# Kernel optimization log

Hardware: AMD Instinct MI355X
Metric: run time of the kernel (lower is better)

Reference implementation:

```python
import jax, jax.numpy as jnp
import numpy as np

N, C, H, W = 4, 256, 128, 128
BLOCK = 8
FWB = H // BLOCK  # feature_size_with_block = 16
N_BBOX = 100
M = N_BBOX * N * FWB * FWB  # 102400 rois


def setup_inputs() -> dict:
    key = jax.random.key(0)
    ks = jax.random.split(key, 6)
    s = 1.0 / np.sqrt(C).astype(np.float32)
    return {
        "feature": jax.random.normal(ks[0], (N, C, H, W), jnp.float32),
        "rois_feature": jax.random.normal(ks[1], (M, C, 1, 1), jnp.float32),
        "W_weight": jax.random.normal(ks[2], (C, C), jnp.float32) * s,
        "b_weight": jnp.zeros((C,), jnp.float32),
        "W_fuse": jax.random.normal(ks[3], (C, C), jnp.float32) * s,
        "b_fuse": jnp.zeros((C,), jnp.float32),
        "W_pw": jax.random.normal(ks[4], (BLOCK * BLOCK, C), jnp.float32) * s,
        "b_pw": jnp.zeros((BLOCK * BLOCK,), jnp.float32),
        "feature_size_with_block": FWB,
    }


def reference(feature, rois_feature, W_weight, b_weight, W_fuse, b_fuse, W_pw, b_pw, feature_size_with_block):
    n, c, h, w = feature.shape
    f = feature_size_with_block
    blk = h // f  # block_size
    m = rois_feature.shape[0]
    n_bbox = m // (n * f * f)

    x = rois_feature[:, :, 0, 0]  # [M, C] (1x1 conv on 1x1 spatial == dense layer)
    feat_w = jax.nn.relu(x @ W_weight.T + b_weight)  # [M, C]
    feat_f = jax.nn.relu(x @ W_fuse.T + b_fuse)      # [M, C]
    point_weight = feat_w @ W_pw.T + b_pw            # [M, B*B]

    # [n_bbox, N, F, F, B, B] -> [N, n_bbox, F, F, B, B]
    pw = point_weight.reshape(n_bbox, n, f, f, blk, blk).transpose(1, 0, 2, 3, 4, 5)
    # feature -> blocks: [N, C, F, B, F, B] -> [N, C, F, F, B, B]
    fb = feature.reshape(n, c, f, blk, f, blk).transpose(0, 1, 2, 4, 3, 5)
    # weighted block-sum without materializing the n_bbox-repeated tensor.
    # torch: sum over (B,B) -> [N,nb,C,F,F], then permute(1,0,3,4,2) -> [nb,N,F,F,C]
    out = jnp.einsum('ncpqab,nkpqab->knpqc', fb, pw)  # [nb, N, F, F, C]
    out = out.reshape(m, c)[:, :, None, None]          # [M, C, 1, 1]
    fused = feat_f[:, :, None, None] + out
    return fused, out
```

## Files before the change

### kernel.cpp

```cpp
#include <hip/hip_runtime.h>

#define NN 4
#define CC 256
#define HH 128
#define FWBv 16
#define BLK 8
#define NBBOX 100
#define MM (NBBOX * NN * FWBv * FWBv)

typedef __attribute__((ext_vector_type(8))) short bf16x8;
typedef __attribute__((ext_vector_type(4))) float f32x4;

__device__ __forceinline__ unsigned short f2bf(float x) {
  union { float f; unsigned int u; } v; v.f = x;
  unsigned int r = v.u + 0x7FFFu + ((v.u >> 16) & 1u);
  return (unsigned short)(r >> 16);
}

__device__ __forceinline__ void async16(const void* g, void* l) {
  __builtin_amdgcn_global_load_lds(
      (__attribute__((address_space(1))) void*)(g),
      (__attribute__((address_space(3))) void*)(l), 16, 0, 0);
}

__global__ __launch_bounds__(256) void k_convert(
    const float* __restrict__ Wf, const float* __restrict__ Ww,
    const float* __restrict__ Wpw,
    unsigned short* __restrict__ oWf, unsigned short* __restrict__ oWw,
    unsigned short* __restrict__ oWpw) {
  int i = blockIdx.x * 256 + threadIdx.x;
  oWf[i] = f2bf(Wf[i]);
  oWw[i] = f2bf(Ww[i]);
  if (i < 64 * 256) oWpw[i] = f2bf(Wpw[i]);
}


__device__ __forceinline__ void stage_w(const unsigned short* __restrict__ Wp,
                                        int kc, unsigned short* buf, int w,
                                        int lane) {
  const int srcs = ((lane & 3) ^ ((lane >> 3) & 3)) * 8;
  const int rr = lane >> 2;
#pragma unroll
  for (int i = 0; i < 4; ++i) {
    const int r0 = w * 64 + i * 16;
    async16(Wp + (size_t)(r0 + rr) * 256 + kc * 32 + srcs, buf + r0 * 32);
  }
}

__device__ __forceinline__ void stage_wpw(const unsigned short* __restrict__ Wpw,
                                          unsigned short* buf, int kc4, int w,
                                          int lane) {
  const int srcs = ((lane & 7) ^ ((lane >> 3) & 7)) * 8;
  const int rr = lane >> 3;
#pragma unroll
  for (int i = 0; i < 2; ++i) {
    const int r0 = w * 16 + i * 8;
    async16(Wpw + (size_t)(r0 + rr) * 256 + kc4 * 64 + srcs, buf + r0 * 64);
  }
}

__device__ __forceinline__ void body16(const unsigned short* buf,
                                       const unsigned short (*xsp)[264],
                                       int kcol, int w, int lr, int quad,
                                       int wslot, f32x4 acc[4][4]) {
  bf16x8 aw[4], bx[4];
#pragma unroll
  for (int nt = 0; nt < 4; ++nt)
    aw[nt] = *(const bf16x8*)&buf[(w * 64 + nt * 16 + lr) * 32 + wslot];
#pragma unroll
  for (int mt = 0; mt < 4; ++mt)
    bx[mt] = *(const bf16x8*)&xsp[mt * 16 + lr][kcol];
#pragma unroll
  for (int mt = 0; mt < 4; ++mt)
#pragma unroll
    for (int nt = 0; nt < 4; ++nt)
      acc[mt][nt] = __builtin_amdgcn_mfma_f32_16x16x32_bf16(
          aw[nt], bx[mt], acc[mt][nt], 0, 0, 0);
}

__global__ __launch_bounds__(256) void k1(
    const float* __restrict__ rois,
    const unsigned short* __restrict__ Wf,
    const unsigned short* __restrict__ Ww,
    const unsigned short* __restrict__ Wpw,
    const float* __restrict__ bf_, const float* __restrict__ bw_,
    const float* __restrict__ bpw_,
    float* __restrict__ fused_slot,
    float* __restrict__ out_slot)
{
  __shared__ __align__(16) unsigned short xs[64][264];
  __shared__ __align__(16) unsigned short bs[2][8192];
  unsigned short* bsf = &bs[0][0];
  const int t = threadIdx.x;
  const int lane = t & 63, w = t >> 6;
  const int lr = lane & 15, quad = lane >> 4;
  const int row_base = blockIdx.x * 64;
  const int wslot = (quad ^ ((lr >> 1) & 3)) << 3;

  stage_w(Wf, 0, &bs[0][0], w, lane);

#pragma unroll
  for (int i = 0; i < 16; ++i) {
    const int elem = (i * 256 + t) * 4;
    const int r = elem >> 8, c = elem & 255;
    const float4 v = *(const float4*)(rois + (size_t)row_base * 256 + elem);
    unsigned int lo = f2bf(v.x) | ((unsigned int)f2bf(v.y) << 16);
    unsigned int hi = f2bf(v.z) | ((unsigned int)f2bf(v.w) << 16);
    *(uint2*)&xs[r][c] = make_uint2(lo, hi);
  }
  asm volatile("s_waitcnt vmcnt(0) lgkmcnt(0)" ::: "memory");
  __builtin_amdgcn_s_barrier();

  f32x4 acc[4][4];
#pragma unroll
  for (int mt = 0; mt < 4; ++mt)
#pragma unroll
    for (int nt = 0; nt < 4; ++nt) acc[mt][nt] = (f32x4){0.f, 0.f, 0.f, 0.f};

#pragma unroll
  for (int kc = 0; kc < 8; ++kc) {
    if (kc < 7) stage_w(Wf, kc + 1, &bs[(kc + 1) & 1][0], w, lane);
    else        stage_w(Ww, 0, &bs[0][0], w, lane);
    asm volatile("s_waitcnt vmcnt(4)" ::: "memory");
    body16(&bs[kc & 1][0], xs, kc * 32 + quad * 8, w, lr, quad, wslot, acc);
  }

#pragma unroll
  for (int nt = 0; nt < 4; ++nt) {
    const int col0 = w * 64 + nt * 16 + quad * 4;
    const float4 b4 = *(const float4*)(bf_ + col0);
#pragma unroll
    for (int mt = 0; mt < 4; ++mt) {
      float4 v;
      v.x = acc[mt][nt][0] + b4.x; v.x = v.x > 0.f ? v.x : 0.f;
      v.y = acc[mt][nt][1] + b4.y; v.y = v.y > 0.f ? v.y : 0.f;
      v.z = acc[mt][nt][2] + b4.z; v.z = v.z > 0.f ? v.z : 0.f;
      v.w = acc[mt][nt][3] + b4.w; v.w = v.w > 0.f ? v.w : 0.f;
      *(float4*)(fused_slot + (size_t)(row_base + mt * 16 + lr) * 256 + col0) = v;
      acc[mt][nt] = (f32x4){0.f, 0.f, 0.f, 0.f};
    }
  }

#pragma unroll
  for (int kc = 0; kc < 8; ++kc) {
    if (kc < 7) {
      stage_w(Ww, kc + 1, &bs[(kc + 1) & 1][0], w, lane);
      asm volatile("s_waitcnt vmcnt(4)" ::: "memory");
    } else {
      asm volatile("s_waitcnt vmcnt(0)" ::: "memory");
    }
    body16(&bs[kc & 1][0], xs, kc * 32 + quad * 8, w, lr, quad, wslot, acc);
  }

  __builtin_amdgcn_s_barrier();

#pragma unroll
  for (int c = 0; c < 4; ++c) stage_wpw(Wpw, bsf + c * 4096, c, w, lane);

#pragma unroll
  for (int nt = 0; nt < 4; ++nt) {
    const int col0 = w * 64 + nt * 16 + quad * 4;
    const float4 b4 = *(const float4*)(bw_ + col0);
#pragma unroll
    for (int mt = 0; mt < 4; ++mt) {
      float v0 = acc[mt][nt][0] + b4.x; v0 = v0 > 0.f ? v0 : 0.f;
      float v1 = acc[mt][nt][1] + b4.y; v1 = v1 > 0.f ? v1 : 0.f;
      float v2 = acc[mt][nt][2] + b4.z; v2 = v2 > 0.f ? v2 : 0.f;
      float v3 = acc[mt][nt][3] + b4.w; v3 = v3 > 0.f ? v3 : 0.f;
      unsigned int lo = f2bf(v0) | ((unsigned int)f2bf(v1) << 16);
      unsigned int hi = f2bf(v2) | ((unsigned int)f2bf(v3) << 16);
      *(uint2*)&xs[mt * 16 + lr][col0] = make_uint2(lo, hi);
    }
  }
  asm volatile("s_waitcnt vmcnt(0) lgkmcnt(0)" ::: "memory");
  __builtin_amdgcn_s_barrier();

  f32x4 acc2[4];
#pragma unroll
  for (int mt = 0; mt < 4; ++mt) acc2[mt] = (f32x4){0.f, 0.f, 0.f, 0.f};
#pragma unroll
  for (int c = 0; c < 4; ++c) {
#pragma unroll
    for (int kt = 0; kt < 2; ++kt) {
      const int sl = ((kt * 4 + quad) ^ (lr & 7)) << 3;
      const bf16x8 apw =
          *(const bf16x8*)&bsf[c * 4096 + (w * 16 + lr) * 64 + sl];
      const int kcol = c * 64 + kt * 32 + quad * 8;
#pragma unroll
      for (int mt = 0; mt < 4; ++mt) {
        const bf16x8 bx = *(const bf16x8*)&xs[mt * 16 + lr][kcol];
        acc2[mt] =
            __builtin_amdgcn_mfma_f32_16x16x32_bf16(apw, bx, acc2[mt], 0, 0, 0);
      }
    }
  }
  {
    const int j0 = w * 16 + quad * 4;
    const float4 bj = *(const float4*)(bpw_ + j0);
#pragma unroll
    for (int mt = 0; mt < 4; ++mt) {
      float4 v;
      v.x = acc2[mt][0] + bj.x;
      v.y = acc2[mt][1] + bj.y;
      v.z = acc2[mt][2] + bj.z;
      v.w = acc2[mt][3] + bj.w;
      *(float4*)(out_slot + (size_t)(row_base + mt * 16 + lr) * 256 + j0) = v;
    }
  }
}

__global__ __launch_bounds__(512) void k2(
    const float* __restrict__ feature,
    float* __restrict__ fused_slot,
    float* __restrict__ out_slot)
{
  __shared__ unsigned short fbuf[256][72];
  __shared__ unsigned short pwb[112][72];
  const int t = threadIdx.x;
  const int lane = t & 63, w = t >> 6;
  const int lr = lane & 15, quad = lane >> 4;
  const int bid = blockIdx.x;
  const int n = bid >> 8, p = (bid >> 4) & 15, q = bid & 15;

  if (t < 432) {
    const int r = 100 + t / 36, cw = t % 36;
    *(unsigned int*)&pwb[r][cw * 2] = 0u;
  }

  for (int pi = t; pi < 2048; pi += 512) {
    const int c = pi >> 3, a = pi & 7;
    const float* fp =
        feature + (((size_t)n * 256 + c) * 128 + p * 8 + a) * 128 + q * 8;
    const float4 v0 = *(const float4*)fp;
    const float4 v1 = *(const float4*)(fp + 4);
    unsigned int u0 = f2bf(v0.x) | ((unsigned int)f2bf(v0.y) << 16);
    unsigned int u1 = f2bf(v0.z) | ((unsigned int)f2bf(v0.w) << 16);
    unsigned int u2 = f2bf(v1.x) | ((unsigned int)f2bf(v1.y) << 16);
    unsigned int u3 = f2bf(v1.z) | ((unsigned int)f2bf(v1.w) << 16);
    *(uint4*)&fbuf[c][a * 8] = make_uint4(u0, u1, u2, u3);
  }

  for (int pi = t; pi < 1600; pi += 512) {
    const int k = pi >> 4, ch = pi & 15;
    const float4 v =
        *(const float4*)(out_slot + (size_t)(bid + k * 1024) * 256 + ch * 4);
    unsigned int lo = f2bf(v.x) | ((unsigned int)f2bf(v.y) << 16);
    unsigned int hi = f2bf(v.z) | ((unsigned int)f2bf(v.w) << 16);
    *(uint2*)&pwb[k][ch * 4] = make_uint2(lo, hi);
  }
  __syncthreads();

  f32x4 acc[7][2];
#pragma unroll
  for (int mt = 0; mt < 7; ++mt)
#pragma unroll
    for (int nt = 0; nt < 2; ++nt) acc[mt][nt] = (f32x4){0.f, 0.f, 0.f, 0.f};
#pragma unroll
  for (int kt = 0; kt < 2; ++kt) {
    const int kk = kt * 32 + quad * 8;
    bf16x8 a[7], b[2];
#pragma unroll
    for (int mt = 0; mt < 7; ++mt)
      a[mt] = *(const bf16x8*)&pwb[mt * 16 + lr][kk];
#pragma unroll
    for (int nt = 0; nt < 2; ++nt)
      b[nt] = *(const bf16x8*)&fbuf[w * 32 + nt * 16 + lr][kk];
#pragma unroll
    for (int mt = 0; mt < 7; ++mt)
#pragma unroll
      for (int nt = 0; nt < 2; ++nt)
        acc[mt][nt] =
            __builtin_amdgcn_mfma_f32_16x16x32_bf16(a[mt], b[nt], acc[mt][nt], 0, 0, 0);
  }

#pragma unroll
  for (int mt = 0; mt < 7; ++mt) {
#pragma unroll
    for (int r = 0; r < 4; ++r) {
      const int k = mt * 16 + quad * 4 + r;
      if (k < 100) {
        const size_t rowoff = (size_t)(bid + k * 1024) * 256;
#pragma unroll
        for (int nt = 0; nt < 2; ++nt) {
          const int c = w * 32 + nt * 16 + lr;
          const float val = acc[mt][nt][r];
          out_slot[rowoff + c] = val;
          fused_slot[rowoff + c] = fused_slot[rowoff + c] + val;
        }
      }
    }
  }
}

extern "C" void kernel_launch(void* const* d_in, const int* in_sizes, int n_in,
                              void* d_out, int out_size, void* d_ws, size_t ws_size,
                              hipStream_t stream) {
  const float* feature = (const float*)d_in[0];
  const float* rois = (const float*)d_in[1];
  const float* Ww = (const float*)d_in[2];
  const float* bw = (const float*)d_in[3];
  const float* Wf = (const float*)d_in[4];
  const float* bfv = (const float*)d_in[5];
  const float* Wpw = (const float*)d_in[6];
  const float* bpw = (const float*)d_in[7];

  unsigned short* wsWf = (unsigned short*)d_ws;
  unsigned short* wsWw = wsWf + 256 * 256;
  unsigned short* wsWpw = wsWw + 256 * 256;

  float* fused_slot = (float*)d_out;
  float* out_slot = fused_slot + (size_t)MM * 256;

  k_convert<<<256, 256, 0, stream>>>(Wf, Ww, Wpw, wsWf, wsWw, wsWpw);
  k1<<<MM / 64, 256, 0, stream>>>(rois, wsWf, wsWw, wsWpw, bfv, bw, bpw,
                                  fused_slot, out_slot);
  k2<<<NN * FWBv * FWBv, 512, 0, stream>>>(feature, fused_slot, out_slot);
}
```

Measured before the change: 466.5 us.

## Stage intermediates as bf16 in out_slot and vectorize k2 epilogue stores

k1 now writes point_weight and relu(fuse) as packed bf16 into the out_slot buffer. Each row of out_slot holds 512 bf16 values, with point weights in the first 64 and feat_f at offset 128. It no longer writes an fp32 fused_slot, which cuts k1's write traffic and k2's read-modify-write of fused. In k2 the MFMA operands are swapped so each lane's results are contiguous along channels, which allows float4 stores to out and fused instead of scalar strided stores. s_setprio hints are wrapped around the MFMA blocks. Risks: feat_f is now rounded to bf16 before being added, which reduces precision, and correctness depends on k2 reading the staged bf16 data before overwriting those rows.

```diff
diff --git a/kernel.cpp b/kernel.cpp
--- a/kernel.cpp
+++ b/kernel.cpp
@@ -15,6 +15,11 @@
   union { float f; unsigned int u; } v; v.f = x;
   unsigned int r = v.u + 0x7FFFu + ((v.u >> 16) & 1u);
   return (unsigned short)(r >> 16);
+}
+
+__device__ __forceinline__ float bfbits2f(unsigned int hi16) {
+  union { float f; unsigned int u; } v; v.u = hi16;
+  return v.f;
 }
 
 __device__ __forceinline__ void async16(const void* g, void* l) {
@@ -70,12 +75,14 @@
 #pragma unroll
   for (int mt = 0; mt < 4; ++mt)
     bx[mt] = *(const bf16x8*)&xsp[mt * 16 + lr][kcol];
+  __builtin_amdgcn_s_setprio(1);
 #pragma unroll
   for (int mt = 0; mt < 4; ++mt)
 #pragma unroll
     for (int nt = 0; nt < 4; ++nt)
       acc[mt][nt] = __builtin_amdgcn_mfma_f32_16x16x32_bf16(
           aw[nt], bx[mt], acc[mt][nt], 0, 0, 0);
+  __builtin_amdgcn_s_setprio(0);
 }
 
 __global__ __launch_bounds__(256) void k1(
@@ -85,12 +92,12 @@
     const unsigned short* __restrict__ Wpw,
     const float* __restrict__ bf_, const float* __restrict__ bw_,
     const float* __restrict__ bpw_,
-    float* __restrict__ fused_slot,
     float* __restrict__ out_slot)
 {
   __shared__ __align__(16) unsigned short xs[64][264];
   __shared__ __align__(16) unsigned short bs[2][8192];
   unsigned short* bsf = &bs[0][0];
+  unsigned short* os = (unsigned short*)out_slot;
   const int t = threadIdx.x;
   const int lane = t & 63, w = t >> 6;
   const int lr = lane & 15, quad = lane >> 4;
@@ -131,12 +138,14 @@
     const float4 b4 = *(const float4*)(bf_ + col0);
 #pragma unroll
     for (int mt = 0; mt < 4; ++mt) {
-      float4 v;
-      v.x = acc[mt][nt][0] + b4.x; v.x = v.x > 0.f ? v.x : 0.f;
-      v.y = acc[mt][nt][1] + b4.y; v.y = v.y > 0.f ? v.y : 0.f;
-      v.z = acc[mt][nt][2] + b4.z; v.z = v.z > 0.f ? v.z : 0.f;
-      v.w = acc[mt][nt][3] + b4.w; v.w = v.w > 0.f ? v.w : 0.f;
-      *(float4*)(fused_slot + (size_t)(row_base + mt * 16 + lr) * 256 + col0) = v;
+      float v0 = acc[mt][nt][0] + b4.x; v0 = v0 > 0.f ? v0 : 0.f;
+      float v1 = acc[mt][nt][1] + b4.y; v1 = v1 > 0.f ? v1 : 0.f;
+      float v2 = acc[mt][nt][2] + b4.z; v2 = v2 > 0.f ? v2 : 0.f;
+      float v3 = acc[mt][nt][3] + b4.w; v3 = v3 > 0.f ? v3 : 0.f;
+      unsigned int lo = f2bf(v0) | ((unsigned int)f2bf(v1) << 16);
+      unsigned int hi = f2bf(v2) | ((unsigned int)f2bf(v3) << 16);
+      *(uint2*)&os[(size_t)(row_base + mt * 16 + lr) * 512 + 128 + col0] =
+          make_uint2(lo, hi);
       acc[mt][nt] = (f32x4){0.f, 0.f, 0.f, 0.f};
     }
   }
@@ -186,12 +195,14 @@
       const bf16x8 apw =
           *(const bf16x8*)&bsf[c * 4096 + (w * 16 + lr) * 64 + sl];
       const int kcol = c * 64 + kt * 32 + quad * 8;
+      __builtin_amdgcn_s_setprio(1);
 #pragma unroll
       for (int mt = 0; mt < 4; ++mt) {
         const bf16x8 bx = *(const bf16x8*)&xs[mt * 16 + lr][kcol];
         acc2[mt] =
             __builtin_amdgcn_mfma_f32_16x16x32_bf16(apw, bx, acc2[mt], 0, 0, 0);
       }
+      __builtin_amdgcn_s_setprio(0);
     }
   }
   {
@@ -199,12 +210,14 @@
     const float4 bj = *(const float4*)(bpw_ + j0);
 #pragma unroll
     for (int mt = 0; mt < 4; ++mt) {
-      float4 v;
-      v.x = acc2[mt][0] + bj.x;
-      v.y = acc2[mt][1] + bj.y;
-      v.z = acc2[mt][2] + bj.z;
-      v.w = acc2[mt][3] + bj.w;
-      *(float4*)(out_slot + (size_t)(row_base + mt * 16 + lr) * 256 + j0) = v;
+      float v0 = acc2[mt][0] + bj.x;
+      float v1 = acc2[mt][1] + bj.y;
+      float v2 = acc2[mt][2] + bj.z;
+      float v3 = acc2[mt][3] + bj.w;
+      unsigned int lo = f2bf(v0) | ((unsigned int)f2bf(v1) << 16);
+      unsigned int hi = f2bf(v2) | ((unsigned int)f2bf(v3) << 16);
+      *(uint2*)&os[(size_t)(row_base + mt * 16 + lr) * 512 + j0] =
+          make_uint2(lo, hi);
     }
   }
 }
@@ -221,6 +234,7 @@
   const int lr = lane & 15, quad = lane >> 4;
   const int bid = blockIdx.x;
   const int n = bid >> 8, p = (bid >> 4) & 15, q = bid & 15;
+  const unsigned short* os = (const unsigned short*)out_slot;
 
   if (t < 432) {
     const int r = 100 + t / 36, cw = t % 36;
@@ -242,51 +256,74 @@
 
   for (int pi = t; pi < 1600; pi += 512) {
     const int k = pi >> 4, ch = pi & 15;
-    const float4 v =
-        *(const float4*)(out_slot + (size_t)(bid + k * 1024) * 256 + ch * 4);
-    unsigned int lo = f2bf(v.x) | ((unsigned int)f2bf(v.y) << 16);
-    unsigned int hi = f2bf(v.z) | ((unsigned int)f2bf(v.w) << 16);
-    *(uint2*)&pwb[k][ch * 4] = make_uint2(lo, hi);
+    const uint2 v = *(const uint2*)&os[(size_t)(bid + k * 1024) * 512 + ch * 4];
+    *(uint2*)&pwb[k][ch * 4] = v;
   }
   __syncthreads();
 
+  uint2 ffp[7][2];
+#pragma unroll
+  for (int kt = 0; kt < 7; ++kt) {
+    const int k = kt * 16 + lr;
+    if (k < 100) {
+      const size_t ro = (size_t)(bid + k * 1024) * 512;
+#pragma unroll
+      for (int ct = 0; ct < 2; ++ct) {
+        const int c0 = w * 32 + ct * 16 + quad * 4;
+        ffp[kt][ct] = *(const uint2*)&os[ro + 128 + c0];
+      }
+    }
+  }
+
   f32x4 acc[7][2];
 #pragma unroll
-  for (int mt = 0; mt < 7; ++mt)
-#pragma unroll
-    for (int nt = 0; nt < 2; ++nt) acc[mt][nt] = (f32x4){0.f, 0.f, 0.f, 0.f};
-#pragma unroll
-  for (int kt = 0; kt < 2; ++kt) {
-    const int kk = kt * 32 + quad * 8;
-    bf16x8 a[7], b[2];
-#pragma unroll
-    for (int mt = 0; mt < 7; ++mt)
-      a[mt] = *(const bf16x8*)&pwb[mt * 16 + lr][kk];
-#pragma unroll
-    for (int nt = 0; nt < 2; ++nt)
-      b[nt] = *(const bf16x8*)&fbuf[w * 32 + nt * 16 + lr][kk];
-#pragma unroll
-    for (int mt = 0; mt < 7; ++mt)
-#pragma unroll
-      for (int nt = 0; nt < 2; ++nt)
-        acc[mt][nt] =
-            __builtin_amdgcn_mfma_f32_16x16x32_bf16(a[mt], b[nt], acc[mt][nt], 0, 0, 0);
-  }
-
-#pragma unroll
-  for (int mt = 0; mt < 7; ++mt) {
-#pragma unroll
-    for (int r = 0; r < 4; ++r) {
-      const int k = mt * 16 + quad * 4 + r;
-      if (k < 100) {
-        const size_t rowoff = (size_t)(bid + k * 1024) * 256;
-#pragma unroll
-        for (int nt = 0; nt < 2; ++nt) {
-          const int c = w * 32 + nt * 16 + lr;
-          const float val = acc[mt][nt][r];
-          out_slot[rowoff + c] = val;
-          fused_slot[rowoff + c] = fused_slot[rowoff + c] + val;
-        }
+  for (int kt = 0; kt < 7; ++kt)
+#pragma unroll
+    for (int ct = 0; ct < 2; ++ct) acc[kt][ct] = (f32x4){0.f, 0.f, 0.f, 0.f};
+#pragma unroll
+  for (int kj = 0; kj < 2; ++kj) {
+    const int kk = kj * 32 + quad * 8;
+    bf16x8 pa[7], fa[2];
+#pragma unroll
+    for (int kt = 0; kt < 7; ++kt)
+      pa[kt] = *(const bf16x8*)&pwb[kt * 16 + lr][kk];
+#pragma unroll
+    for (int ct = 0; ct < 2; ++ct)
+      fa[ct] = *(const bf16x8*)&fbuf[w * 32 + ct * 16 + lr][kk];
+    __builtin_amdgcn_s_setprio(1);
+#pragma unroll
+    for (int kt = 0; kt < 7; ++kt)
+#pragma unroll
+      for (int ct = 0; ct < 2; ++ct)
+        acc[kt][ct] = __builtin_amdgcn_mfma_f32_16x16x32_bf16(
+            fa[ct], pa[kt], acc[kt][ct], 0, 0, 0);
+    __builtin_amdgcn_s_setprio(0);
+  }
+
+  asm volatile("s_waitcnt vmcnt(0)" ::: "memory");
+  __builtin_amdgcn_s_barrier();
+
+#pragma unroll
+  for (int kt = 0; kt < 7; ++kt) {
+    const int k = kt * 16 + lr;
+    if (k < 100) {
+      const size_t ro = (size_t)(bid + k * 1024) * 256;
+#pragma unroll
+      for (int ct = 0; ct < 2; ++ct) {
+        const int c0 = w * 32 + ct * 16 + quad * 4;
+        float4 v;
+        v.x = acc[kt][ct][0];
+        v.y = acc[kt][ct][1];
+        v.z = acc[kt][ct][2];
+        v.w = acc[kt][ct][3];
+        *(float4*)(out_slot + ro + c0) = v;
+        const uint2 ff = ffp[kt][ct];
+        float4 f;
+        f.x = v.x + bfbits2f(ff.x << 16);
+        f.y = v.y + bfbits2f(ff.x & 0xffff0000u);
+        f.z = v.z + bfbits2f(ff.y << 16);
+        f.w = v.w + bfbits2f(ff.y & 0xffff0000u);
+        *(float4*)(fused_slot + ro + c0) = f;
       }
     }
   }
@@ -313,6 +350,6 @@
 
   k_convert<<<256, 256, 0, stream>>>(Wf, Ww, Wpw, wsWf, wsWw, wsWpw);
   k1<<<MM / 64, 256, 0, stream>>>(rois, wsWf, wsWw, wsWpw, bfv, bw, bpw,
-                                  fused_slot, out_slot);
+                                  out_slot);
   k2<<<NN * FWBv * FWBv, 512, 0, stream>>>(feature, fused_slot, out_slot);
 }
```

New measurement: 455.8 us. 1.02x faster.
